# Optimization experiments

Hardware: AMD Instinct MI355X
Metric: run time of the kernel (lower is better)

The kernel has to match this reference:

```python
import jax, jax.numpy as jnp
import numpy as np

SIDE = 64; EMB = 16; CH = 64; K = 64; V = 64; L = 8
N = SIDE * SIDE

def _pos_table(side, d):
    pe = np.array([[p / np.power(10000, 2 * (j // 2) / d) for j in range(d)]
                   if p != 0 else np.zeros(d) for p in range(side)])
    pe[1:, 0::2] = np.sin(pe[1:, 0::2])
    pe[1:, 1::2] = np.cos(pe[1:, 1::2])
    return pe.astype(np.float32)  # [side, d]

def _pos_emb():
    # Replicates torch .view(1, emb, side, 1): plain reshape of [side, emb] -> [emb, side]
    t = _pos_table(SIDE, EMB).reshape(EMB, SIDE)
    xe = np.broadcast_to(t[:, :, None], (EMB, SIDE, SIDE))
    ye = np.broadcast_to(t[:, None, :], (EMB, SIDE, SIDE))
    return jnp.asarray(np.concatenate([xe, ye], 0).reshape(1, 2 * EMB, N))

def _conv_mask():
    # CausalConv mask, see_center=False, 5x5: zero center pixel onward in center row, and all rows below
    m = np.ones((CH, 3, 5, 5), np.float32)
    m[:, :, 2, 2:] = 0.0
    m[:, :, 3:, :] = 0.0
    return jnp.asarray(m)

def _lrelu(x):
    return jnp.where(x >= 0, x, 0.01 * x)  # LeakyReLU(0.01)

def _bn(x, g, b, eps=1e-5):
    # training-mode batch norm (biased variance), channel axis = 1
    axes = (0,) + tuple(range(2, x.ndim))
    m = jnp.mean(x, axes, keepdims=True)
    var = jnp.mean((x - m) ** 2, axes, keepdims=True)
    sh = (1, -1) + (1,) * (x.ndim - 2)
    return g.reshape(sh) * (x - m) / jnp.sqrt(var + eps) + b.reshape(sh)

def _cv1(w, b, x):
    # 1x1 Conv1d: [O,I] x [B,I,N] -> [B,O,N]
    return jnp.einsum('oi,bin->bon', w, x) + b[:, None]

def reference(x, conv_w, conv_b, bn0_g, bn0_b, q_w, q_b, fk_w, fk_b, ck_w, ck_b,
              fv_w, fv_b, cv_w, cv_b, bn_g, bn_b, out_w, out_b):
    B = x.shape[0]
    pos = jnp.broadcast_to(_pos_emb(), (B, 2 * EMB, N))
    mask = jnp.tril(jnp.ones((N, N), jnp.float32))

    # masked causal conv input layer + BN + LeakyReLU
    w = conv_w * _conv_mask()
    h = jax.lax.conv_general_dilated(x, w, (1, 1), [(2, 2), (2, 2)],
                                     dimension_numbers=('NCHW', 'OIHW', 'NCHW'))
    h = h + conv_b[None, :, None, None]
    h = _lrelu(_bn(h, bn0_g, bn0_b)).reshape(B, CH, N)

    k0 = jnp.zeros((B, K, N), x.dtype)
    v0 = jnp.zeros((B, V, N), x.dtype)
    inv_sqrt_k = 1.0 / jnp.sqrt(jnp.float32(K))

    def layer(carry, p):
        h, k, v = carry
        qw, qb, fkw, fkb, ckw, ckb, fvw, fvb, cvw, cvb, g, bb = p
        x0 = jnp.concatenate([h, pos], 1)            # [B, CH+32, N]
        x0k = jnp.concatenate([x0, k], 1)            # [B, 160, N]
        x0v = jnp.concatenate([x0, v], 1)
        fk = jax.nn.sigmoid(_cv1(fkw, fkb, x0k))
        ck = _lrelu(_cv1(ckw, ckb, x0k))
        k_new = fk * k + ck                          # highway-gated persistent K
        fv = jax.nn.sigmoid(_cv1(fvw, fvb, x0v))
        cv_ = _lrelu(_cv1(cvw, cvb, x0v))
        v_new = fv * v + cv_
        q = _lrelu(_cv1(qw, qb, x0))                 # [B, K, N]
        attn = jnp.einsum('bkn,bkm->bnm', q, k) * inv_sqrt_k  # uses OLD k
        attn = attn * mask + (1.0 - mask) * (-10000.0)
        attn = jax.nn.softmax(attn, axis=-1) * mask
        out1 = jnp.einsum('bnm,bvm->bvn', attn, v)   # uses OLD v; [B, V, N]
        # original code computes fc(out1) but discards it (out2 overwritten)
        h2 = _lrelu(_bn(out1, g, bb))
        return (h2, k_new, v_new), None

    params = (q_w, q_b, fk_w, fk_b, ck_w, ck_b, fv_w, fv_b, cv_w, cv_b, bn_g, bn_b)
    (h, k, v), _ = jax.lax.scan(layer, (h, k0, v0), params)

    out = jnp.einsum('oi,bin->bon', out_w, h) + out_b[None, :, None]
    return out.reshape(B, out_w.shape[0], SIDE, SIDE)

def setup_inputs() -> dict:
    key = jax.random.key(0)
    ks = jax.random.split(key, 12)
    s = 0.05
    return {
        'x': jax.random.normal(ks[0], (2, 3, 64, 64), jnp.float32),
        'conv_w': jax.random.normal(ks[1], (CH, 3, 5, 5), jnp.float32) * s,
        'conv_b': jnp.zeros((CH,), jnp.float32),
        'bn0_g': jnp.ones((CH,), jnp.float32),
        'bn0_b': jnp.zeros((CH,), jnp.float32),
        'q_w': jax.random.normal(ks[2], (L, K, CH + 2 * EMB), jnp.float32) * s,
        'q_b': jnp.zeros((L, K), jnp.float32),
        'fk_w': jax.random.normal(ks[3], (L, K, CH + K + 2 * EMB), jnp.float32) * s,
        'fk_b': jnp.zeros((L, K), jnp.float32),
        'ck_w': jax.random.normal(ks[4], (L, K, CH + K + 2 * EMB), jnp.float32) * s,
        'ck_b': jnp.zeros((L, K), jnp.float32),
        'fv_w': jax.random.normal(ks[5], (L, V, CH + V + 2 * EMB), jnp.float32) * s,
        'fv_b': jnp.zeros((L, V), jnp.float32),
        'cv_w': jax.random.normal(ks[6], (L, V, CH + V + 2 * EMB), jnp.float32) * s,
        'cv_b': jnp.zeros((L, V), jnp.float32),
        'bn_g': jnp.ones((L, CH), jnp.float32),
        'bn_b': jnp.zeros((L, CH), jnp.float32),
        'out_w': jax.random.normal(ks[7], (100, V), jnp.float32) * s,
        'out_b': jnp.zeros((100,), jnp.float32),
    }
```

## Files before the change

kernel.cpp:

```cpp
#include <hip/hip_runtime.h>

#define NPIX 4096
#define CHN  64

typedef __attribute__((ext_vector_type(8))) short short8;
typedef __attribute__((ext_vector_type(8))) unsigned short ushort8;
typedef __attribute__((ext_vector_type(4))) unsigned short ushort4v;
typedef __attribute__((ext_vector_type(4))) float f32x4;
typedef __attribute__((ext_vector_type(16))) float f32x16;
typedef __attribute__((ext_vector_type(4))) unsigned int uint4v;

__device__ __forceinline__ float lrelu_(float x){ return x >= 0.f ? x : 0.01f*x; }

__device__ __forceinline__ unsigned short f2bf(float x){
  union { float f; unsigned u; } v; v.f = x;
  unsigned r = v.u + 0x7FFF + ((v.u >> 16) & 1);
  return (unsigned short)(r >> 16);
}
__device__ __forceinline__ float bf2f(unsigned short h){
  union { unsigned u; float f; } v; v.u = ((unsigned)h) << 16;
  return v.f;
}
__device__ __forceinline__ float asf_(unsigned u){
  union { unsigned u; float f; } v; v.u = u; return v.f;
}

__global__ void pos_kernel(float* __restrict__ pos){
  int idx = blockIdx.x*256 + threadIdx.x;
  int c = idx >> 12;
  int n = idx & (NPIX-1);
  int bcoord = (c < 16) ? (n >> 6) : (n & 63);
  int a = (c < 16) ? c : (c - 16);
  int flat = a*64 + bcoord;
  int p = flat >> 4;
  int j = flat & 15;
  float val = 0.f;
  if (p != 0){
    float ex = (float)(j & ~1) * (1.f/16.f);
    float w = powf(10000.f, -ex);
    float ang = (float)p * w;
    val = (j & 1) ? cosf(ang) : sinf(ang);
  }
  pos[idx] = val;
}

__global__ void wtr_kernel(const float* __restrict__ qw, const float* __restrict__ fkw,
                           const float* __restrict__ ckw, const float* __restrict__ fvw,
                           const float* __restrict__ cvw, const float* __restrict__ convw,
                           float* __restrict__ wt){
  int idx = blockIdx.x*256 + threadIdx.x;
  if (idx >= 381632) return;
  if (idx < 49152){
    int l = idx / 6144, r = idx % 6144, i = r >> 6, o = r & 63;
    wt[idx] = qw[(l*64 + o)*96 + i];
  } else if (idx < 376832){
    int e = idx - 49152;
    int mat = e / 81920, r = e % 81920;
    int l = r / 10240, rr = r % 10240, i = rr >> 6, o = rr & 63;
    const float* src = (mat==0) ? fkw : (mat==1) ? ckw : (mat==2) ? fvw : cvw;
    wt[idx] = src[(l*64 + o)*160 + i];
  } else {
    int e = idx - 376832;
    int o = e & 63, tap = e >> 6;
    int ci = tap / 25, r = tap % 25;
    wt[idx] = convw[(o*3 + ci)*25 + r];
  }
}

__global__ __launch_bounds__(256) void conv_in_kernel(const float* __restrict__ x,
                                                      const float* __restrict__ cwt,
                                                      const float* __restrict__ cb,
                                                      float* __restrict__ out){
  int t = threadIdx.x;
  int o = t & 63;
  int sub = t >> 6;
  int bid = blockIdx.x;
  int b = bid >> 10;
  int n = ((bid & 1023) << 2) + sub;
  int y = n >> 6, xx = n & 63;
  float acc = cb[o];
  #pragma unroll
  for (int ci=0; ci<3; ++ci){
    const float* xp = x + ((b*3+ci)<<12);
    #pragma unroll
    for (int ky=0; ky<3; ++ky){
      int yy = y + ky - 2;
      if (yy < 0) continue;
      int nk = (ky==2) ? 2 : 5;
      #pragma unroll
      for (int kx=0; kx<5; ++kx){
        if (kx >= nk) break;
        int xc = xx + kx - 2;
        if (xc < 0 || xc > 63) continue;
        acc += xp[(yy<<6) + xc] * cwt[(ci*25 + ky*5 + kx)*64 + o];
      }
    }
  }
  out[(b*CHN+o)*NPIX + n] = acc;
}

__global__ __launch_bounds__(1024) void bn_stats_kernel(const float* __restrict__ xin,
                                                        float* __restrict__ stats){
  int c = blockIdx.x;
  int t = threadIdx.x;
  float s = 0.f, ss = 0.f;
  #pragma unroll
  for (int it=0; it<8; ++it){
    int idx = t + it*1024;
    float v = xin[(((idx>>12))*CHN + c)*NPIX + (idx & (NPIX-1))];
    s += v; ss += v*v;
  }
  #pragma unroll
  for (int o=1; o<64; o<<=1){ s += __shfl_xor(s,o); ss += __shfl_xor(ss,o); }
  __shared__ float ps[16], pq[16];
  if ((t & 63) == 0){ ps[t>>6] = s; pq[t>>6] = ss; }
  __syncthreads();
  if (t == 0){
    float S=0.f, Q=0.f;
    #pragma unroll
    for (int i=0;i<16;++i){ S += ps[i]; Q += pq[i]; }
    float mu = S*(1.f/8192.f);
    float var = Q*(1.f/8192.f) - mu*mu;
    var = fmaxf(var, 0.f);
    stats[c*2]   = mu;
    stats[c*2+1] = rsqrtf(var + 1e-5f);
  }
}

__global__ void bn_apply_kernel(const float* __restrict__ xin, const float* __restrict__ stats,
                                const float* __restrict__ g, const float* __restrict__ bb,
                                float* __restrict__ hout){
  int idx = blockIdx.x*256 + threadIdx.x;
  int e = idx << 2;
  int c = (e >> 12) & 63;
  float mu = stats[c*2], rstd = stats[c*2+1];
  float gain = g[c]*rstd;
  float beta = bb[c] - gain*mu;
  float4 v = *(const float4*)(xin + e);
  float4 r;
  r.x = lrelu_(gain*v.x + beta);
  r.y = lrelu_(gain*v.y + beta);
  r.z = lrelu_(gain*v.z + beta);
  r.w = lrelu_(gain*v.w + beta);
  *(float4*)(hout + e) = r;
}

__global__ __launch_bounds__(256) void bn_apply2_kernel(float* __restrict__ hbuf,
                                                        const float* __restrict__ psum,
                                                        const float* __restrict__ psq,
                                                        const float* __restrict__ g,
                                                        const float* __restrict__ bb){
  int bid = blockIdx.x;
  int ebase = bid << 10;
  int c = (ebase >> 12) & 63;
  int t = threadIdx.x;
  float s = psum[c*256 + t];
  float q = psq[c*256 + t];
  #pragma unroll
  for (int o=1; o<64; o<<=1){ s += __shfl_xor(s,o); q += __shfl_xor(q,o); }
  __shared__ float as[4], aq[4];
  if ((t & 63) == 0){ as[t>>6] = s; aq[t>>6] = q; }
  __syncthreads();
  float S = as[0]+as[1]+as[2]+as[3];
  float Q = aq[0]+aq[1]+aq[2]+aq[3];
  float mu = S*(1.f/8192.f);
  float var = fmaxf(Q*(1.f/8192.f) - mu*mu, 0.f);
  float rstd = rsqrtf(var + 1e-5f);
  float gain = g[c]*rstd;
  float beta = bb[c] - gain*mu;
  float4 v = *(const float4*)(hbuf + ebase + t*4);
  float4 r;
  r.x = lrelu_(gain*v.x + beta);
  r.y = lrelu_(gain*v.y + beta);
  r.z = lrelu_(gain*v.z + beta);
  r.w = lrelu_(gain*v.w + beta);
  *(float4*)(hbuf + ebase + t*4) = r;
}

__global__ __launch_bounds__(256) void cv1_kernel(
    const float* __restrict__ hbuf, const float* __restrict__ pos,
    const float* __restrict__ kold,
    const unsigned short* __restrict__ vhTo, const unsigned short* __restrict__ vlTo,
    const float* __restrict__ qwt,
    const float* __restrict__ fkwt, const float* __restrict__ ckwt,
    const float* __restrict__ fvwt, const float* __restrict__ cvwt,
    const float* __restrict__ qbi,  const float* __restrict__ fkb,
    const float* __restrict__ ckb,  const float* __restrict__ fvb,
    const float* __restrict__ cvb,
    unsigned short* __restrict__ qh, unsigned short* __restrict__ ql,
    float* __restrict__ knew, unsigned short* __restrict__ khn, unsigned short* __restrict__ kln,
    unsigned short* __restrict__ vhTn, unsigned short* __restrict__ vlTn)
{
  int t = threadIdx.x;
  int o  = t & 63;
  int wv = t >> 6;
  int b    = blockIdx.x >> 8;
  int tile = blockIdx.x & 255;
  int n0 = tile*16 + wv*4;

  const float* hb = hbuf + b*CHN*NPIX + n0;
  const float* kb = kold + b*CHN*NPIX + n0;
  const unsigned short* vhb_ = vhTo + (size_t)(b*CHN)*NPIX + n0;
  const unsigned short* vlb_ = vlTo + (size_t)(b*CHN)*NPIX + n0;
  const float* pb = pos + n0;

  auto load4 = [&](const float* p, float* dst){
    float4 a = *(const float4*)p;
    dst[0]=a.x; dst[1]=a.y; dst[2]=a.z; dst[3]=a.w;
  };

  float x[4];
  long obase = (long)(b*CHN+o)*NPIX + n0;
  size_t nbase = ((size_t)b*NPIX + n0)*64 + o;

  {
    float aq[4];
    float bias = qbi[o];
    #pragma unroll
    for (int j=0;j<4;++j) aq[j]=bias;
    #pragma unroll 4
    for (int i=0;i<64;++i){
      load4(hb + i*NPIX, x);
      float w = qwt[i*64 + o];
      #pragma unroll
      for (int j=0;j<4;++j) aq[j] += w*x[j];
    }
    #pragma unroll 4
    for (int i=0;i<32;++i){
      load4(pb + i*NPIX, x);
      float w = qwt[(64+i)*64 + o];
      #pragma unroll
      for (int j=0;j<4;++j) aq[j] += w*x[j];
    }
    #pragma unroll
    for (int j=0;j<4;++j){
      float v = lrelu_(aq[j]) * (0.125f * 1.4426950408889634f);
      unsigned short hb16 = f2bf(v);
      qh[nbase + (size_t)j*64] = hb16;
      ql[nbase + (size_t)j*64] = f2bf(v - bf2f(hb16));
    }
  }

  {
    float af[4], ac[4];
    float bf = fkb[o], bc = ckb[o];
    #pragma unroll
    for (int j=0;j<4;++j){ af[j]=bf; ac[j]=bc; }
    #pragma unroll 4
    for (int i=0;i<64;++i){
      load4(hb + i*NPIX, x);
      float wf = fkwt[i*64+o], wc = ckwt[i*64+o];
      #pragma unroll
      for (int j=0;j<4;++j){ af[j] += wf*x[j]; ac[j] += wc*x[j]; }
    }
    #pragma unroll 4
    for (int i=0;i<32;++i){
      load4(pb + i*NPIX, x);
      float wf = fkwt[(64+i)*64+o], wc = ckwt[(64+i)*64+o];
      #pragma unroll
      for (int j=0;j<4;++j){ af[j] += wf*x[j]; ac[j] += wc*x[j]; }
    }
    #pragma unroll 4
    for (int i=0;i<64;++i){
      load4(kb + i*NPIX, x);
      float wf = fkwt[(96+i)*64+o], wc = ckwt[(96+i)*64+o];
      #pragma unroll
      for (int j=0;j<4;++j){ af[j] += wf*x[j]; ac[j] += wc*x[j]; }
    }
    float kv[4];
    load4(kb + o*NPIX, kv);
    #pragma unroll
    for (int j=0;j<4;++j){
      float fk = 1.f/(1.f+__expf(-af[j]));
      float kn = fk*kv[j] + lrelu_(ac[j]);
      knew[obase+j] = kn;
      unsigned short hb16 = f2bf(kn);
      khn[nbase + (size_t)j*64] = hb16;
      kln[nbase + (size_t)j*64] = f2bf(kn - bf2f(hb16));
    }
  }

  {
    float af[4], ac[4];
    float bf = fvb[o], bc = cvb[o];
    #pragma unroll
    for (int j=0;j<4;++j){ af[j]=bf; ac[j]=bc; }
    #pragma unroll 4
    for (int i=0;i<64;++i){
      load4(hb + i*NPIX, x);
      float wf = fvwt[i*64+o], wc = cvwt[i*64+o];
      #pragma unroll
      for (int j=0;j<4;++j){ af[j] += wf*x[j]; ac[j] += wc*x[j]; }
    }
    #pragma unroll 4
    for (int i=0;i<32;++i){
      load4(pb + i*NPIX, x);
      float wf = fvwt[(64+i)*64+o], wc = cvwt[(64+i)*64+o];
      #pragma unroll
      for (int j=0;j<4;++j){ af[j] += wf*x[j]; ac[j] += wc*x[j]; }
    }
    #pragma unroll 4
    for (int i=0;i<64;++i){
      ushort4v xh = *(const ushort4v*)(vhb_ + (size_t)i*NPIX);
      ushort4v xl = *(const ushort4v*)(vlb_ + (size_t)i*NPIX);
      float wf = fvwt[(96+i)*64+o], wc = cvwt[(96+i)*64+o];
      #pragma unroll
      for (int j=0;j<4;++j){
        float xv = bf2f(xh[j]) + bf2f(xl[j]);
        af[j] += wf*xv; ac[j] += wc*xv;
      }
    }
    ushort4v vvh = *(const ushort4v*)(vhb_ + (size_t)o*NPIX);
    ushort4v vvl = *(const ushort4v*)(vlb_ + (size_t)o*NPIX);
    ushort4v vph, vpl;
    #pragma unroll
    for (int j=0;j<4;++j){
      float fv = 1.f/(1.f+__expf(-af[j]));
      float vold_ = bf2f(vvh[j]) + bf2f(vvl[j]);
      float vn = fv*vold_ + lrelu_(ac[j]);
      unsigned short hb16 = f2bf(vn);
      vph[j] = hb16;
      vpl[j] = f2bf(vn - bf2f(hb16));
    }
    *(ushort4v*)(vhTn + ((size_t)(b*CHN+o))*NPIX + n0) = vph;
    *(ushort4v*)(vlTn + ((size_t)(b*CHN+o))*NPIX + n0) = vpl;
  }
}

__device__ __forceinline__ void pack_sf(const f32x16& sfv, unsigned (&ph)[4][2],
                                        unsigned (&pl)[4][2]){
  #pragma unroll
  for (int a=0; a<4; ++a){
    unsigned h0, h1;
    asm("v_cvt_pk_bf16_f32 %0, %1, %2" : "=v"(h0) : "v"(sfv[4*a]),   "v"(sfv[4*a+1]));
    asm("v_cvt_pk_bf16_f32 %0, %1, %2" : "=v"(h1) : "v"(sfv[4*a+2]), "v"(sfv[4*a+3]));
    float r0 = sfv[4*a]   - asf_(h0 << 16);
    float r1 = sfv[4*a+1] - asf_(h0 & 0xffff0000u);
    float r2 = sfv[4*a+2] - asf_(h1 << 16);
    float r3 = sfv[4*a+3] - asf_(h1 & 0xffff0000u);
    unsigned l0, l1;
    asm("v_cvt_pk_bf16_f32 %0, %1, %2" : "=v"(l0) : "v"(r0), "v"(r1));
    asm("v_cvt_pk_bf16_f32 %0, %1, %2" : "=v"(l1) : "v"(r2), "v"(r3));
    ph[a][0]=h0; ph[a][1]=h1; pl[a][0]=l0; pl[a][1]=l1;
  }
}

__global__ __launch_bounds__(128) void attn_mfma(
    const unsigned short* __restrict__ qhg, const unsigned short* __restrict__ qlg,
    const unsigned short* __restrict__ khg, const unsigned short* __restrict__ klg,
    const unsigned short* __restrict__ vhg, const unsigned short* __restrict__ vlg,
    float* __restrict__ part)
{
  int bid = 1087 - (int)blockIdx.x;
  int b = 0, id = bid;
  if (id >= 544){ b = 1; id -= 544; }
  int pidx = bid;
  int rem = id, k = 0;
  while (rem >= 4*(k+1)){ rem -= 4*(k+1); ++k; }
  int rt    = 4*k + rem/(k+1);
  int chunk = rem - (rem/(k+1))*(k+1);

  int C0  = chunk << 8;
  int end = min(C0 + 256, rt*64 + 64);
  int nt  = (end - C0 + 63) >> 6;

  int t = threadIdx.x;
  int w = t >> 6;
  int l = t & 63;
  int q = l & 31;
  int hi = l >> 5;
  int qbase = rt*64 + w*32;
  int n_g = qbase + q;
  int nmax_w = qbase + 31;

  __shared__ __align__(16) char KH[8192], KL[8192];
  __shared__ __align__(16) char VH[8192], VL[8192];

  const unsigned short* qhp = qhg + (size_t)b*NPIX*64;
  const unsigned short* qlp = qlg + (size_t)b*NPIX*64;
  const unsigned short* khp = khg + (size_t)b*NPIX*64;
  const unsigned short* klp = klg + (size_t)b*NPIX*64;
  const unsigned short* vhp = vhg + (size_t)b*CHN*NPIX;
  const unsigned short* vlp = vlg + (size_t)b*CHN*NPIX;

  short8 qhf[4], qlf[4];
  #pragma unroll
  for (int kc=0; kc<4; ++kc){
    qhf[kc] = *(const short8*)(qhp + (size_t)n_g*64 + kc*16 + hi*8);
    qlf[kc] = *(const short8*)(qlp + (size_t)n_g*64 + kc*16 + hi*8);
  }

  int srow[4], scc8[4], soff[4];
  #pragma unroll
  for (int p=0; p<4; ++p){
    int slot = t + (p<<7);
    int row = slot >> 3, cc = slot & 7;
    srow[p] = row; scc8[p] = cc*8;
    soff[p] = row*128 + ((cc ^ (row & 7)) << 4);
  }
  ushort8 rkh[4], rkl[4], rvh[4], rvl[4];
  auto issue = [&](int m0){
    #pragma unroll
    for (int p=0; p<4; ++p){
      rkh[p] = *(const ushort8*)(khp + (size_t)(m0+srow[p])*64 + scc8[p]);
      rkl[p] = *(const ushort8*)(klp + (size_t)(m0+srow[p])*64 + scc8[p]);
      rvh[p] = *(const ushort8*)(vhp + (size_t)srow[p]*NPIX + m0 + scc8[p]);
      rvl[p] = *(const ushort8*)(vlp + (size_t)srow[p]*NPIX + m0 + scc8[p]);
    }
  };

  f32x16 oacc0, oacc1;
  #pragma unroll
  for (int i=0; i<16; ++i){ oacc0[i]=0.f; oacc1[i]=0.f; }
  float m_run = -1e30f, l_run = 0.f;

  issue(C0);
  for (int ti=0; ti<nt; ++ti){
    int m0 = C0 + (ti<<6);
    __syncthreads();
    #pragma unroll
    for (int p=0; p<4; ++p){
      *(ushort8*)(KH + soff[p]) = rkh[p];
      *(ushort8*)(KL + soff[p]) = rkl[p];
      *(ushort8*)(VH + soff[p]) = rvh[p];
      *(ushort8*)(VL + soff[p]) = rvl[p];
    }
    __syncthreads();
    if (ti+1 < nt) issue(m0 + 64);

    if (m0 <= nmax_w){
      f32x16 sf0, sf1;
      #pragma unroll
      for (int i=0; i<16; ++i){ sf0[i]=0.f; sf1[i]=0.f; }
      #pragma unroll
      for (int kc=0; kc<4; ++kc){
        int off0 = q*128 + (((2*kc + hi) ^ (q & 7)) << 4);
        short8 ah0 = *(const short8*)(KH + off0);
        short8 al0 = *(const short8*)(KL + off0);
        short8 ah1 = *(const short8*)(KH + off0 + 4096);
        short8 al1 = *(const short8*)(KL + off0 + 4096);
        sf0 = __builtin_amdgcn_mfma_f32_32x32x16_bf16(ah0, qhf[kc], sf0, 0,0,0);
        sf1 = __builtin_amdgcn_mfma_f32_32x32x16_bf16(ah1, qhf[kc], sf1, 0,0,0);
        sf0 = __builtin_amdgcn_mfma_f32_32x32x16_bf16(al0, qhf[kc], sf0, 0,0,0);
        sf1 = __builtin_amdgcn_mfma_f32_32x32x16_bf16(al1, qhf[kc], sf1, 0,0,0);
        sf0 = __builtin_amdgcn_mfma_f32_32x32x16_bf16(ah0, qlf[kc], sf0, 0,0,0);
        sf1 = __builtin_amdgcn_mfma_f32_32x32x16_bf16(ah1, qlf[kc], sf1, 0,0,0);
      }
      float mx = -1e30f;
      #pragma unroll
      for (int r=0; r<16; ++r){
        int mg0 = m0 + (r&3) + 8*(r>>2) + 4*hi;
        float s0 = (mg0 <= n_g) ? sf0[r] : -1e30f;
        float s1 = (mg0 + 32 <= n_g) ? sf1[r] : -1e30f;
        sf0[r] = s0; sf1[r] = s1;
        mx = fmaxf(mx, fmaxf(s0, s1));
      }
      mx = fmaxf(mx, __shfl_xor(mx, 32));
      float m_new = fmaxf(m_run, mx);
      float alpha = exp2f(m_run - m_new);
      float ps = 0.f;
      #pragma unroll
      for (int r=0; r<16; ++r){
        float e0 = exp2f(sf0[r] - m_new);
        float e1 = exp2f(sf1[r] - m_new);
        sf0[r] = e0; sf1[r] = e1;
        ps += e0 + e1;
      }
      ps += __shfl_xor(ps, 32);
      l_run = l_run*alpha + ps;
      m_run = m_new;

      unsigned ph0[4][2], pl0[4][2], ph1[4][2], pl1[4][2];
      pack_sf(sf0, ph0, pl0);
      pack_sf(sf1, ph1, pl1);

      #pragma unroll
      for (int i=0; i<16; ++i){ oacc0[i] *= alpha; oacc1[i] *= alpha; }

#define PV_KC(KC, PH, PL) { \
      const int kk = (KC)&1; \
      unsigned oh0 = hi ? PH[2*kk+1][0] : PH[2*kk][0]; \
      unsigned oh1 = hi ? PH[2*kk+1][1] : PH[2*kk][1]; \
      unsigned sh0 = hi ? PH[2*kk][0]   : PH[2*kk+1][0]; \
      unsigned sh1 = hi ? PH[2*kk][1]   : PH[2*kk+1][1]; \
      unsigned rh0 = __shfl_xor(sh0, 32); \
      unsigned rh1 = __shfl_xor(sh1, 32); \
      unsigned ol0 = hi ? PL[2*kk+1][0] : PL[2*kk][0]; \
      unsigned ol1 = hi ? PL[2*kk+1][1] : PL[2*kk][1]; \
      unsigned sl0 = hi ? PL[2*kk][0]   : PL[2*kk+1][0]; \
      unsigned sl1 = hi ? PL[2*kk][1]   : PL[2*kk+1][1]; \
      unsigned rl0 = __shfl_xor(sl0, 32); \
      unsigned rl1 = __shfl_xor(sl1, 32); \
      union { uint4v u; short8 s; } fh, fl; \
      fh.u[0] = hi ? rh0 : oh0; fh.u[1] = hi ? rh1 : oh1; \
      fh.u[2] = hi ? oh0 : rh0; fh.u[3] = hi ? oh1 : rh1; \
      fl.u[0] = hi ? rl0 : ol0; fl.u[1] = hi ? rl1 : ol1; \
      fl.u[2] = hi ? ol0 : rl0; fl.u[3] = hi ? ol1 : rl1; \
      int poff = q*128 + (((2*(KC) + hi) ^ (q & 7)) << 4); \
      short8 xvh0 = *(const short8*)(VH + poff); \
      short8 xvl0 = *(const short8*)(VL + poff); \
      short8 xvh1 = *(const short8*)(VH + poff + 4096); \
      short8 xvl1 = *(const short8*)(VL + poff + 4096); \
      oacc0 = __builtin_amdgcn_mfma_f32_32x32x16_bf16(xvh0, fh.s, oacc0, 0,0,0); \
      oacc1 = __builtin_amdgcn_mfma_f32_32x32x16_bf16(xvh1, fh.s, oacc1, 0,0,0); \
      oacc0 = __builtin_amdgcn_mfma_f32_32x32x16_bf16(xvl0, fh.s, oacc0, 0,0,0); \
      oacc1 = __builtin_amdgcn_mfma_f32_32x32x16_bf16(xvl1, fh.s, oacc1, 0,0,0); \
      oacc0 = __builtin_amdgcn_mfma_f32_32x32x16_bf16(xvh0, fl.s, oacc0, 0,0,0); \
      oacc1 = __builtin_amdgcn_mfma_f32_32x32x16_bf16(xvh1, fl.s, oacc1, 0,0,0); \
    }
      PV_KC(0, ph0, pl0)
      PV_KC(1, ph0, pl0)
      PV_KC(2, ph1, pl1)
      PV_KC(3, ph1, pl1)
#undef PV_KC
    }
  }

  float* pacc = part + (size_t)pidx * 4224;
  #pragma unroll
  for (int vf=0; vf<2; ++vf){
    #pragma unroll
    for (int qd=0; qd<4; ++qd){
      int vd = 32*vf + 8*qd + 4*hi;
      f32x4 vv;
      vv.x = vf ? oacc1[4*qd]   : oacc0[4*qd];
      vv.y = vf ? oacc1[4*qd+1] : oacc0[4*qd+1];
      vv.z = vf ? oacc1[4*qd+2] : oacc0[4*qd+2];
      vv.w = vf ? oacc1[4*qd+3] : oacc0[4*qd+3];
      *(f32x4*)(pacc + (size_t)(w*32 + q)*64 + vd) = vv;
    }
  }
  if (l < 32){
    pacc[4096 + (w*32 + l)*2]     = m_run;
    pacc[4096 + (w*32 + l)*2 + 1] = l_run;
  }
}

__global__ __launch_bounds__(256) void attn_combine(const float* __restrict__ part,
                                                    float* __restrict__ out1,
                                                    float* __restrict__ psum,
                                                    float* __restrict__ psq){
  int bid = blockIdx.x;
  int b = bid >> 7, rt = bid & 127;
  int rt64 = rt >> 1;
  int g2 = rt64 >> 2;
  int nch = g2 + 1;
  int base = b*544 + 2*g2*(g2+1) + (rt64 & 3)*(g2+1);

  int t = threadIdx.x;
  int nl = t & 31, vq = t >> 5;
  int row64 = (rt & 1)*32 + nl;

  float M = -1e30f;
  #pragma unroll
  for (int c=0; c<16; ++c)
    if (c < nch) M = fmaxf(M, part[(size_t)(base+c)*4224 + 4096 + row64*2]);

  float L = 0.f;
  float val[8];
  #pragma unroll
  for (int jj=0; jj<8; ++jj) val[jj] = 0.f;
  #pragma unroll
  for (int c=0; c<16; ++c){
    if (c < nch){
      const float* pa = part + (size_t)(base+c)*4224;
      float wgt = exp2f(pa[4096 + row64*2] - M);
      L += pa[4096 + row64*2 + 1] * wgt;
      #pragma unroll
      for (int jj=0; jj<8; ++jj) val[jj] += wgt * pa[row64*64 + vq*8 + jj];
    }
  }
  float invL = 1.f / L;
  float s[8], q[8];
  #pragma unroll
  for (int jj=0; jj<8; ++jj){
    float v = val[jj]*invL;
    out1[((size_t)b*CHN + vq*8 + jj)*NPIX + rt*32 + nl] = v;
    s[jj] = v; q[jj] = v*v;
  }
  #pragma unroll
  for (int o2=1; o2<32; o2<<=1){
    #pragma unroll
    for (int jj=0; jj<8; ++jj){
      s[jj] += __shfl_xor(s[jj], o2);
      q[jj] += __shfl_xor(q[jj], o2);
    }
  }
  if (nl == 0){
    #pragma unroll
    for (int jj=0; jj<8; ++jj){
      int c = vq*8 + jj;
      psum[c*256 + bid] = s[jj];
      psq [c*256 + bid] = q[jj];
    }
  }
}

__global__ __launch_bounds__(256) void final_kernel(const float* __restrict__ h,
                                                    const float* __restrict__ ow,
                                                    const float* __restrict__ ob,
                                                    float* __restrict__ out){
  int idx = blockIdx.x*256 + threadIdx.x;
  int b  = idx / 409600;
  int r  = idx - b*409600;
  int oc = r >> 12;
  int n  = r & (NPIX-1);
  const float* hp = h + (size_t)b*CHN*NPIX + n;
  const float* wp = ow + oc*64;
  float acc = ob[oc];
  #pragma unroll
  for (int v=0; v<64; ++v) acc += wp[v]*hp[(size_t)v*NPIX];
  out[idx] = acc;
}

extern "C" void kernel_launch(void* const* d_in, const int* in_sizes, int n_in,
                              void* d_out, int out_size, void* d_ws, size_t ws_size,
                              hipStream_t stream){
  const float* x     = (const float*)d_in[0];
  const float* convw = (const float*)d_in[1];
  const float* convb = (const float*)d_in[2];
  const float* bn0g  = (const float*)d_in[3];
  const float* bn0b  = (const float*)d_in[4];
  const float* qw    = (const float*)d_in[5];
  const float* qbias = (const float*)d_in[6];
  const float* fkw   = (const float*)d_in[7];
  const float* fkb   = (const float*)d_in[8];
  const float* ckw   = (const float*)d_in[9];
  const float* ckb   = (const float*)d_in[10];
  const float* fvw   = (const float*)d_in[11];
  const float* fvb   = (const float*)d_in[12];
  const float* cvw   = (const float*)d_in[13];
  const float* cvb   = (const float*)d_in[14];
  const float* bng   = (const float*)d_in[15];
  const float* bnb   = (const float*)d_in[16];
  const float* ow    = (const float*)d_in[17];
  const float* ob    = (const float*)d_in[18];

  const size_t TEN = (size_t)2*CHN*NPIX;
  const size_t BFU = TEN/2;
  float* ws   = (float*)d_ws;
  float* pos  = ws;
  float* h    = pos + 32*NPIX;
  float* k0   = h  + TEN;
  float* k1   = k0 + TEN;
  float* stats = k1 + TEN;
  float* psum = stats + 128;
  float* psq  = psum + 64*256;
  float* wt   = psq + 64*256;
  float* bfb  = wt + 381632;
  unsigned short* qh  = (unsigned short*)(bfb);
  unsigned short* ql  = (unsigned short*)(bfb + BFU);
  unsigned short* kh0 = (unsigned short*)(bfb + 2*BFU);
  unsigned short* kh1 = (unsigned short*)(bfb + 3*BFU);
  unsigned short* kl0 = (unsigned short*)(bfb + 4*BFU);
  unsigned short* kl1 = (unsigned short*)(bfb + 5*BFU);
  unsigned short* vh0 = (unsigned short*)(bfb + 6*BFU);
  unsigned short* vh1 = (unsigned short*)(bfb + 7*BFU);
  unsigned short* vl0 = (unsigned short*)(bfb + 8*BFU);
  unsigned short* vl1 = (unsigned short*)(bfb + 9*BFU);
  float* part = bfb + 10*BFU;

  hipMemsetAsync(k0, 0, TEN*sizeof(float), stream);
  hipMemsetAsync(kh0, 0, TEN*2, stream);
  hipMemsetAsync(kl0, 0, TEN*2, stream);
  hipMemsetAsync(vh0, 0, TEN*2, stream);
  hipMemsetAsync(vl0, 0, TEN*2, stream);

  pos_kernel<<<512,256,0,stream>>>(pos);
  wtr_kernel<<<1491,256,0,stream>>>(qw, fkw, ckw, fvw, cvw, convw, wt);
  conv_in_kernel<<<2048,256,0,stream>>>(x, wt + 376832, convb, h);
  bn_stats_kernel<<<64,1024,0,stream>>>(h, stats);
  bn_apply_kernel<<<512,256,0,stream>>>(h, stats, bn0g, bn0b, h);

  float* kfp[2] = {k0,k1};
  unsigned short* khb[2] = {kh0,kh1};
  unsigned short* klb[2] = {kl0,kl1};
  unsigned short* vhb[2] = {vh0,vh1};
  unsigned short* vlb[2] = {vl0,vl1};
  for (int l=0; l<8; ++l){
    float* kold = kfp[l&1]; float* knew = kfp[(l+1)&1];
    cv1_kernel<<<512,256,0,stream>>>(h, pos, kold, vhb[l&1], vlb[l&1],
        wt + l*6144,
        wt + 49152 + l*10240,
        wt + 49152 + 81920 + l*10240,
        wt + 49152 + 2*81920 + l*10240,
        wt + 49152 + 3*81920 + l*10240,
        qbias + l*64, fkb + l*64, ckb + l*64, fvb + l*64, cvb + l*64,
        qh, ql,
        knew, khb[(l+1)&1], klb[(l+1)&1],
        vhb[(l+1)&1], vlb[(l+1)&1]);
    attn_mfma<<<1088,128,0,stream>>>(qh, ql, khb[l&1], klb[l&1], vhb[l&1], vlb[l&1], part);
    attn_combine<<<256,256,0,stream>>>(part, h, psum, psq);
    bn_apply2_kernel<<<512,256,0,stream>>>(h, psum, psq, bng + l*64, bnb + l*64);
  }
  final_kernel<<<3200,256,0,stream>>>(h, ow, ob, (float*)d_out);
}
```

Measured before the change: 898.5 us.

## Interleave gate weights, keep fp32 V state, halve pixels per thread in cv1

```diff
diff --git a/kernel.cpp b/kernel.cpp
--- a/kernel.cpp
+++ b/kernel.cpp
@@ -6,6 +6,7 @@
 typedef __attribute__((ext_vector_type(8))) short short8;
 typedef __attribute__((ext_vector_type(8))) unsigned short ushort8;
 typedef __attribute__((ext_vector_type(4))) unsigned short ushort4v;
+typedef __attribute__((ext_vector_type(2))) unsigned short ushort2v;
 typedef __attribute__((ext_vector_type(4))) float f32x4;
 typedef __attribute__((ext_vector_type(16))) float f32x16;
 typedef __attribute__((ext_vector_type(4))) unsigned int uint4v;
@@ -55,9 +56,11 @@
     wt[idx] = qw[(l*64 + o)*96 + i];
   } else if (idx < 376832){
     int e = idx - 49152;
-    int mat = e / 81920, r = e % 81920;
-    int l = r / 10240, rr = r % 10240, i = rr >> 6, o = rr & 63;
-    const float* src = (mat==0) ? fkw : (mat==1) ? ckw : (mat==2) ? fvw : cvw;
+    int grp = e / 163840, r = e % 163840;
+    int l = r / 20480, rr = r % 20480;
+    int i = rr >> 7, rest = rr & 127;
+    int o = rest >> 1, sel = rest & 1;
+    const float* src = (grp==0) ? (sel==0 ? fkw : ckw) : (sel==0 ? fvw : cvw);
     wt[idx] = src[(l*64 + o)*160 + i];
   } else {
     int e = idx - 376832;
@@ -179,151 +182,127 @@
 
 __global__ __launch_bounds__(256) void cv1_kernel(
     const float* __restrict__ hbuf, const float* __restrict__ pos,
-    const float* __restrict__ kold,
-    const unsigned short* __restrict__ vhTo, const unsigned short* __restrict__ vlTo,
+    const float* __restrict__ kold, const float* __restrict__ vold,
     const float* __restrict__ qwt,
-    const float* __restrict__ fkwt, const float* __restrict__ ckwt,
-    const float* __restrict__ fvwt, const float* __restrict__ cvwt,
+    const float* __restrict__ fkck, const float* __restrict__ fvcv,
     const float* __restrict__ qbi,  const float* __restrict__ fkb,
     const float* __restrict__ ckb,  const float* __restrict__ fvb,
     const float* __restrict__ cvb,
     unsigned short* __restrict__ qh, unsigned short* __restrict__ ql,
     float* __restrict__ knew, unsigned short* __restrict__ khn, unsigned short* __restrict__ kln,
-    unsigned short* __restrict__ vhTn, unsigned short* __restrict__ vlTn)
+    float* __restrict__ vnew, unsigned short* __restrict__ vhTn, unsigned short* __restrict__ vlTn)
 {
   int t = threadIdx.x;
   int o  = t & 63;
   int wv = t >> 6;
-  int b    = blockIdx.x >> 8;
-  int tile = blockIdx.x & 255;
-  int n0 = tile*16 + wv*4;
+  int b    = blockIdx.x >> 9;
+  int tile = blockIdx.x & 511;
+  int n0 = tile*8 + wv*2;
 
   const float* hb = hbuf + b*CHN*NPIX + n0;
   const float* kb = kold + b*CHN*NPIX + n0;
-  const unsigned short* vhb_ = vhTo + (size_t)(b*CHN)*NPIX + n0;
-  const unsigned short* vlb_ = vlTo + (size_t)(b*CHN)*NPIX + n0;
+  const float* vb = vold + b*CHN*NPIX + n0;
   const float* pb = pos + n0;
 
-  auto load4 = [&](const float* p, float* dst){
-    float4 a = *(const float4*)p;
-    dst[0]=a.x; dst[1]=a.y; dst[2]=a.z; dst[3]=a.w;
-  };
-
-  float x[4];
   long obase = (long)(b*CHN+o)*NPIX + n0;
   size_t nbase = ((size_t)b*NPIX + n0)*64 + o;
 
   {
-    float aq[4];
     float bias = qbi[o];
-    #pragma unroll
-    for (int j=0;j<4;++j) aq[j]=bias;
-    #pragma unroll 4
+    float a0 = bias, a1 = bias;
+    #pragma unroll 8
     for (int i=0;i<64;++i){
-      load4(hb + i*NPIX, x);
+      float2 xv = *(const float2*)(hb + i*NPIX);
       float w = qwt[i*64 + o];
-      #pragma unroll
-      for (int j=0;j<4;++j) aq[j] += w*x[j];
-    }
-    #pragma unroll 4
+      a0 += w*xv.x; a1 += w*xv.y;
+    }
+    #pragma unroll 8
     for (int i=0;i<32;++i){
-      load4(pb + i*NPIX, x);
+      float2 xv = *(const float2*)(pb + i*NPIX);
       float w = qwt[(64+i)*64 + o];
-      #pragma unroll
-      for (int j=0;j<4;++j) aq[j] += w*x[j];
-    }
-    #pragma unroll
-    for (int j=0;j<4;++j){
-      float v = lrelu_(aq[j]) * (0.125f * 1.4426950408889634f);
-      unsigned short hb16 = f2bf(v);
-      qh[nbase + (size_t)j*64] = hb16;
-      ql[nbase + (size_t)j*64] = f2bf(v - bf2f(hb16));
-    }
+      a0 += w*xv.x; a1 += w*xv.y;
+    }
+    const float QS = 0.125f * 1.4426950408889634f;
+    float v0_ = lrelu_(a0)*QS, v1_ = lrelu_(a1)*QS;
+    unsigned short h0 = f2bf(v0_), h1 = f2bf(v1_);
+    qh[nbase]    = h0;
+    qh[nbase+64] = h1;
+    ql[nbase]    = f2bf(v0_ - bf2f(h0));
+    ql[nbase+64] = f2bf(v1_ - bf2f(h1));
   }
 
   {
-    float af[4], ac[4];
-    float bf = fkb[o], bc = ckb[o];
-    #pragma unroll
-    for (int j=0;j<4;++j){ af[j]=bf; ac[j]=bc; }
-    #pragma unroll 4
+    float af0 = fkb[o], af1 = af0;
+    float ac0 = ckb[o], ac1 = ac0;
+    #pragma unroll 8
     for (int i=0;i<64;++i){
-      load4(hb + i*NPIX, x);
-      float wf = fkwt[i*64+o], wc = ckwt[i*64+o];
-      #pragma unroll
-      for (int j=0;j<4;++j){ af[j] += wf*x[j]; ac[j] += wc*x[j]; }
-    }
-    #pragma unroll 4
+      float2 xv = *(const float2*)(hb + i*NPIX);
+      float2 w = *(const float2*)(fkck + i*128 + o*2);
+      af0 += w.x*xv.x; af1 += w.x*xv.y;
+      ac0 += w.y*xv.x; ac1 += w.y*xv.y;
+    }
+    #pragma unroll 8
     for (int i=0;i<32;++i){
-      load4(pb + i*NPIX, x);
-      float wf = fkwt[(64+i)*64+o], wc = ckwt[(64+i)*64+o];
-      #pragma unroll
-      for (int j=0;j<4;++j){ af[j] += wf*x[j]; ac[j] += wc*x[j]; }
-    }
-    #pragma unroll 4
+      float2 xv = *(const float2*)(pb + i*NPIX);
+      float2 w = *(const float2*)(fkck + (64+i)*128 + o*2);
+      af0 += w.x*xv.x; af1 += w.x*xv.y;
+      ac0 += w.y*xv.x; ac1 += w.y*xv.y;
+    }
+    #pragma unroll 8
     for (int i=0;i<64;++i){
-      load4(kb + i*NPIX, x);
-      float wf = fkwt[(96+i)*64+o], wc = ckwt[(96+i)*64+o];
-      #pragma unroll
-      for (int j=0;j<4;++j){ af[j] += wf*x[j]; ac[j] += wc*x[j]; }
-    }
-    float kv[4];
-    load4(kb + o*NPIX, kv);
-    #pragma unroll
-    for (int j=0;j<4;++j){
-      float fk = 1.f/(1.f+__expf(-af[j]));
-      float kn = fk*kv[j] + lrelu_(ac[j]);
-      knew[obase+j] = kn;
-      unsigned short hb16 = f2bf(kn);
-      khn[nbase + (size_t)j*64] = hb16;
-      kln[nbase + (size_t)j*64] = f2bf(kn - bf2f(hb16));
-    }
+      float2 xv = *(const float2*)(kb + i*NPIX);
+      float2 w = *(const float2*)(fkck + (96+i)*128 + o*2);
+      af0 += w.x*xv.x; af1 += w.x*xv.y;
+      ac0 += w.y*xv.x; ac1 += w.y*xv.y;
+    }
+    float2 kv = *(const float2*)(kb + o*NPIX);
+    float fk0 = 1.f/(1.f+__expf(-af0));
+    float fk1 = 1.f/(1.f+__expf(-af1));
+    float kn0 = fk0*kv.x + lrelu_(ac0);
+    float kn1 = fk1*kv.y + lrelu_(ac1);
+    *(float2*)(knew + obase) = make_float2(kn0, kn1);
+    unsigned short h0 = f2bf(kn0), h1 = f2bf(kn1);
+    khn[nbase]    = h0;
+    khn[nbase+64] = h1;
+    kln[nbase]    = f2bf(kn0 - bf2f(h0));
+    kln[nbase+64] = f2bf(kn1 - bf2f(h1));
   }
 
   {
-    float af[4], ac[4];
-    float bf = fvb[o], bc = cvb[o];
-    #pragma unroll
-    for (int j=0;j<4;++j){ af[j]=bf; ac[j]=bc; }
-    #pragma unroll 4
+    float af0 = fvb[o], af1 = af0;
+    float ac0 = cvb[o], ac1 = ac0;
+    #pragma unroll 8
     for (int i=0;i<64;++i){
-      load4(hb + i*NPIX, x);
-      float wf = fvwt[i*64+o], wc = cvwt[i*64+o];
-      #pragma unroll
-      for (int j=0;j<4;++j){ af[j] += wf*x[j]; ac[j] += wc*x[j]; }
-    }
-    #pragma unroll 4
+      float2 xv = *(const float2*)(hb + i*NPIX);
+      float2 w = *(const float2*)(fvcv + i*128 + o*2);
+      af0 += w.x*xv.x; af1 += w.x*xv.y;
+      ac0 += w.y*xv.x; ac1 += w.y*xv.y;
+    }
+    #pragma unroll 8
     for (int i=0;i<32;++i){
-      load4(pb + i*NPIX, x);
-      float wf = fvwt[(64+i)*64+o], wc = cvwt[(64+i)*64+o];
-      #pragma unroll
-      for (int j=0;j<4;++j){ af[j] += wf*x[j]; ac[j] += wc*x[j]; }
-    }
-    #pragma unroll 4
+      float2 xv = *(const float2*)(pb + i*NPIX);
+      float2 w = *(const float2*)(fvcv + (64+i)*128 + o*2);
+      af0 += w.x*xv.x; af1 += w.x*xv.y;
+      ac0 += w.y*xv.x; ac1 += w.y*xv.y;
+    }
+    #pragma unroll 8
     for (int i=0;i<64;++i){
-      ushort4v xh = *(const ushort4v*)(vhb_ + (size_t)i*NPIX);
-      ushort4v xl = *(const ushort4v*)(vlb_ + (size_t)i*NPIX);
-      float wf = fvwt[(96+i)*64+o], wc = cvwt[(96+i)*64+o];
-      #pragma unroll
-      for (int j=0;j<4;++j){
-        float xv = bf2f(xh[j]) + bf2f(xl[j]);
-        af[j] += wf*xv; ac[j] += wc*xv;
-      }
-    }
-    ushort4v vvh = *(const ushort4v*)(vhb_ + (size_t)o*NPIX);
-    ushort4v vvl = *(const ushort4v*)(vlb_ + (size_t)o*NPIX);
-    ushort4v vph, vpl;
-    #pragma unroll
-    for (int j=0;j<4;++j){
-      float fv = 1.f/(1.f+__expf(-af[j]));
-      float vold_ = bf2f(vvh[j]) + bf2f(vvl[j]);
-      float vn = fv*vold_ + lrelu_(ac[j]);
-      unsigned short hb16 = f2bf(vn);
-      vph[j] = hb16;
-      vpl[j] = f2bf(vn - bf2f(hb16));
-    }
-    *(ushort4v*)(vhTn + ((size_t)(b*CHN+o))*NPIX + n0) = vph;
-    *(ushort4v*)(vlTn + ((size_t)(b*CHN+o))*NPIX + n0) = vpl;
+      float2 xv = *(const float2*)(vb + i*NPIX);
+      float2 w = *(const float2*)(fvcv + (96+i)*128 + o*2);
+      af0 += w.x*xv.x; af1 += w.x*xv.y;
+      ac0 += w.y*xv.x; ac1 += w.y*xv.y;
+    }
+    float2 vv = *(const float2*)(vb + o*NPIX);
+    float fv0 = 1.f/(1.f+__expf(-af0));
+    float fv1 = 1.f/(1.f+__expf(-af1));
+    float vn0 = fv0*vv.x + lrelu_(ac0);
+    float vn1 = fv1*vv.y + lrelu_(ac1);
+    *(float2*)(vnew + obase) = make_float2(vn0, vn1);
+    unsigned short h0 = f2bf(vn0), h1 = f2bf(vn1);
+    ushort2v vph = {h0, h1};
+    ushort2v vpl = {f2bf(vn0 - bf2f(h0)), f2bf(vn1 - bf2f(h1))};
+    *(ushort2v*)(vhTn + ((size_t)(b*CHN+o))*NPIX + n0) = vph;
+    *(ushort2v*)(vlTn + ((size_t)(b*CHN+o))*NPIX + n0) = vpl;
   }
 }
 
@@ -643,7 +622,9 @@
   float* h    = pos + 32*NPIX;
   float* k0   = h  + TEN;
   float* k1   = k0 + TEN;
-  float* stats = k1 + TEN;
+  float* v0   = k1 + TEN;
+  float* v1   = v0 + TEN;
+  float* stats = v1 + TEN;
   float* psum = stats + 128;
   float* psq  = psum + 64*256;
   float* wt   = psq + 64*256;
@@ -661,6 +642,7 @@
   float* part = bfb + 10*BFU;
 
   hipMemsetAsync(k0, 0, TEN*sizeof(float), stream);
+  hipMemsetAsync(v0, 0, TEN*sizeof(float), stream);
   hipMemsetAsync(kh0, 0, TEN*2, stream);
   hipMemsetAsync(kl0, 0, TEN*2, stream);
   hipMemsetAsync(vh0, 0, TEN*2, stream);
@@ -673,22 +655,22 @@
   bn_apply_kernel<<<512,256,0,stream>>>(h, stats, bn0g, bn0b, h);
 
   float* kfp[2] = {k0,k1};
+  float* vfp[2] = {v0,v1};
   unsigned short* khb[2] = {kh0,kh1};
   unsigned short* klb[2] = {kl0,kl1};
   unsigned short* vhb[2] = {vh0,vh1};
   unsigned short* vlb[2] = {vl0,vl1};
   for (int l=0; l<8; ++l){
     float* kold = kfp[l&1]; float* knew = kfp[(l+1)&1];
-    cv1_kernel<<<512,256,0,stream>>>(h, pos, kold, vhb[l&1], vlb[l&1],
+    float* vold = vfp[l&1]; float* vnew = vfp[(l+1)&1];
+    cv1_kernel<<<1024,256,0,stream>>>(h, pos, kold, vold,
         wt + l*6144,
-        wt + 49152 + l*10240,
-        wt + 49152 + 81920 + l*10240,
-        wt + 49152 + 2*81920 + l*10240,
-        wt + 49152 + 3*81920 + l*10240,
+        wt + 49152 + l*20480,
+        wt + 49152 + 163840 + l*20480,
         qbias + l*64, fkb + l*64, ckb + l*64, fvb + l*64, cvb + l*64,
         qh, ql,
         knew, khb[(l+1)&1], klb[(l+1)&1],
-        vhb[(l+1)&1], vlb[(l+1)&1]);
+        vnew, vhb[(l+1)&1], vlb[(l+1)&1]);
     attn_mfma<<<1088,128,0,stream>>>(qh, ql, khb[l&1], klb[l&1], vhb[l&1], vlb[l&1], part);
     attn_combine<<<256,256,0,stream>>>(part, h, psum, psq);
     bn_apply2_kernel<<<512,256,0,stream>>>(h, psum, psq, bng + l*64, bnb + l*64);
```

Result: slower. 1.278 ms (+42.2%).
